# Performance work log

Measured on AMD Instinct MI355X. Metric: run time of the kernel, lower is better.

## Reference

```python
import jax, jax.numpy as jnp
import numpy as np

B, T, P, L, H = 65536, 256, 4, 14, 32
IN = P + L  # 18


def setup_inputs() -> dict:
    key = jax.random.key(0)
    ks = jax.random.split(key, 8)
    s1 = 1.0 / np.sqrt(IN)
    s2 = 1.0 / np.sqrt(H)
    return {
        "phys": jax.random.normal(ks[0], (B, T, P), dtype=jnp.float32),
        "latents": jax.random.normal(ks[1], (B, L), dtype=jnp.float32),
        "W1": jax.random.uniform(ks[2], (IN, H), jnp.float32, -s1, s1),
        "b1": jax.random.uniform(ks[3], (H,), jnp.float32, -s1, s1),
        "W2": jax.random.uniform(ks[4], (H, H), jnp.float32, -s2, s2),
        "b2": jax.random.uniform(ks[5], (H,), jnp.float32, -s2, s2),
        "W3": jax.random.uniform(ks[6], (H, L), jnp.float32, -s2, s2),
        "b3": jax.random.uniform(ks[7], (L,), jnp.float32, -s2, s2),
    }


def reference(phys, latents, W1, b1, W2, b2, W3, b3):
    # phys: [B, T, P]; latents: [B, L]. Dropout p=0.0 -> identity (eval-equivalent).
    phys_t = jnp.swapaxes(phys, 0, 1)  # [T, B, P] for scan over time

    def step(lat, ph):
        x = jnp.concatenate([ph, lat], axis=1)          # [B, P+L]
        h = jax.nn.relu(x @ W1 + b1)                    # [B, H]
        h = jax.nn.relu(h @ W2 + b2)                    # [B, H]
        lat = lat + (h @ W3 + b3)                       # residual update [B, L]
        return lat, lat

    _, outs = jax.lax.scan(step, latents, phys_t)       # outs: [T, B, L]
    return jnp.swapaxes(outs, 0, 1)                     # [B, T, L]
```

## Files before the change

### kernel.cpp

```cpp
#include <hip/hip_runtime.h>


#define BB 65536
#define TT 256
#define LL 14
#define HH 32

typedef float f32x16 __attribute__((ext_vector_type(16)));
typedef __bf16 bf16x8 __attribute__((ext_vector_type(8)));
typedef int i32x2 __attribute__((ext_vector_type(2)));

static __device__ __forceinline__ void split2(float v0, float v1,
                                              unsigned& hw, unsigned& lw) {
    unsigned u0 = __float_as_uint(v0), u1 = __float_as_uint(v1);
    unsigned h0 = (u0 + 0x8000u) & 0xFFFF0000u;
    unsigned h1 = (u1 + 0x8000u) & 0xFFFF0000u;
    float l0 = v0 - __uint_as_float(h0);
    float l1 = v1 - __uint_as_float(h1);
    unsigned s0 = __float_as_uint(l0), s1 = __float_as_uint(l1);
    hw = (h0 >> 16) | h1;
    lw = ((s0 + 0x8000u) >> 16) | ((s1 + 0x8000u) & 0xFFFF0000u);
}

static __device__ __forceinline__ bf16x8 mkfrag(unsigned w0, unsigned w1,
                                                unsigned w2, unsigned w3) {
    union { unsigned u[4]; bf16x8 v; } x;
    x.u[0] = w0; x.u[1] = w1; x.u[2] = w2; x.u[3] = w3;
    return x.v;
}

static __device__ __forceinline__ f32x16 mf(bf16x8 a, bf16x8 b, f32x16 c) {
    return __builtin_amdgcn_mfma_f32_32x32x16_bf16(a, b, c, 0, 0, 0);
}

#if __has_builtin(__builtin_amdgcn_permlane32_swap)
static __device__ __forceinline__ void xswap(unsigned a, unsigned b,
                                             unsigned& a_out, unsigned& b_out) {
    i32x2 r = __builtin_amdgcn_permlane32_swap((int)a, (int)b, false, false);
    a_out = (unsigned)r[0];
    b_out = (unsigned)r[1];
}
#else
static __device__ __forceinline__ void xswap(unsigned a, unsigned b,
                                             unsigned& a_out, unsigned& b_out) {
    const int lane = threadIdx.x & 63;
    const int idx = (lane ^ 32) << 2;
    unsigned sa = (unsigned)__builtin_amdgcn_ds_bpermute(idx, (int)a);
    unsigned sb = (unsigned)__builtin_amdgcn_ds_bpermute(idx, (int)b);
    const bool hi = lane >= 32;
    a_out = hi ? sb : a;
    b_out = hi ? b : sa;
}
#endif

static __device__ __forceinline__ void hfrag(const f32x16& h,
                                             bf16x8& B0h, bf16x8& B0l,
                                             bf16x8& B1h, bf16x8& B1l) {
    unsigned Wh[8], Wl[8];
#pragma unroll
    for (int p = 0; p < 8; ++p) split2(h[2 * p], h[2 * p + 1], Wh[p], Wl[p]);
    unsigned a02h, b02h, a02l, b02l, a13h, b13h, a13l, b13l;
    xswap(Wh[0], Wh[2], a02h, b02h); xswap(Wl[0], Wl[2], a02l, b02l);
    xswap(Wh[1], Wh[3], a13h, b13h); xswap(Wl[1], Wl[3], a13l, b13l);
    B0h = mkfrag(a02h, a13h, b02h, b13h);
    B0l = mkfrag(a02l, a13l, b02l, b13l);
    unsigned a46h, b46h, a46l, b46l, a57h, b57h, a57l, b57l;
    xswap(Wh[4], Wh[6], a46h, b46h); xswap(Wl[4], Wl[6], a46l, b46l);
    xswap(Wh[5], Wh[7], a57h, b57h); xswap(Wl[5], Wl[7], a57l, b57l);
    B1h = mkfrag(a46h, a57h, b46h, b57h);
    B1l = mkfrag(a46l, a57l, b46l, b57l);
}

__global__ __launch_bounds__(256, 2)
void emulator_kernel(const float* __restrict__ phys,
                     const float* __restrict__ latents,
                     const float* __restrict__ W1g,
                     const float* __restrict__ b1g,
                     const float* __restrict__ W2g,
                     const float* __restrict__ b2g,
                     const float* __restrict__ W3g,
                     const float* __restrict__ b3g,
                     float* __restrict__ out) {
    const int tid = threadIdx.x;
    const int lane = tid & 63;
    const int wv = tid >> 6;
    const int c = lane & 31;
    const bool hi = lane >= 32;
    const int kb = hi ? 8 : 0;
    const int r = blockIdx.x * 128 + wv * 32 + c;

    bf16x8 A1t0h, A1t0l, A1c;
    {
        unsigned hw[4], lw[4];
#pragma unroll
        for (int w = 0; w < 4; ++w) {
            const int k0 = kb + 2 * w;
            split2(W1g[k0 * HH + c], W1g[(k0 + 1) * HH + c], hw[w], lw[w]);
        }
        A1t0h = mkfrag(hw[0], hw[1], hw[2], hw[3]);
        A1t0l = mkfrag(lw[0], lw[1], lw[2], lw[3]);
        unsigned whp, wlp;
        split2(W1g[16 * HH + c], W1g[17 * HH + c], whp, wlp);
        A1c = hi ? mkfrag(0, 0, 0, 0) : mkfrag(whp, whp, wlp, 0);
    }
    bf16x8 A2h0, A2l0, A2h1, A2l1, A3h0, A3l0, A3h1, A3l1;
    {
        unsigned hw[4], lw[4];
#pragma unroll
        for (int w = 0; w < 4; ++w) {
            const int k0 = kb + 2 * w;
            split2(W2g[k0 * HH + c], W2g[(k0 + 1) * HH + c], hw[w], lw[w]);
        }
        A2h0 = mkfrag(hw[0], hw[1], hw[2], hw[3]);
        A2l0 = mkfrag(lw[0], lw[1], lw[2], lw[3]);
#pragma unroll
        for (int w = 0; w < 4; ++w) {
            const int k0 = 16 + kb + 2 * w;
            split2(W2g[k0 * HH + c], W2g[(k0 + 1) * HH + c], hw[w], lw[w]);
        }
        A2h1 = mkfrag(hw[0], hw[1], hw[2], hw[3]);
        A2l1 = mkfrag(lw[0], lw[1], lw[2], lw[3]);
#pragma unroll
        for (int w = 0; w < 4; ++w) {
            const int k0 = kb + 2 * w;
            const float e0 = (c < LL) ? W3g[k0 * LL + c] : 0.0f;
            const float e1 = (c < LL) ? W3g[(k0 + 1) * LL + c] : 0.0f;
            split2(e0, e1, hw[w], lw[w]);
        }
        A3h0 = mkfrag(hw[0], hw[1], hw[2], hw[3]);
        A3l0 = mkfrag(lw[0], lw[1], lw[2], lw[3]);
#pragma unroll
        for (int w = 0; w < 4; ++w) {
            const int k0 = 16 + kb + 2 * w;
            const float e0 = (c < LL) ? W3g[k0 * LL + c] : 0.0f;
            const float e1 = (c < LL) ? W3g[(k0 + 1) * LL + c] : 0.0f;
            split2(e0, e1, hw[w], lw[w]);
        }
        A3h1 = mkfrag(hw[0], hw[1], hw[2], hw[3]);
        A3l1 = mkfrag(lw[0], lw[1], lw[2], lw[3]);
    }

    f32x16 cb1, cb2, cb3;
#pragma unroll
    for (int rr = 0; rr < 16; ++rr) {
        const int row = (rr & 3) + 8 * (rr >> 2) + (hi ? 4 : 0);
        cb1[rr] = b1g[row];
        cb2[rr] = b2g[row];
        cb3[rr] = (row < LL) ? b3g[row] : 0.0f;
    }

    f32x16 lat;
#pragma unroll
    for (int i = 0; i < 16; ++i) lat[i] = 0.0f;
    {
        const float* lrow = latents + (size_t)r * LL;
        const float2* p01 = reinterpret_cast<const float2*>(lrow + (hi ? 4 : 0));
        const float2 v0 = p01[0], v1 = p01[1];
        lat[0] = v0.x; lat[1] = v0.y; lat[2] = v1.x; lat[3] = v1.y;
        const float2 v2 = reinterpret_cast<const float2*>(lrow + (hi ? 12 : 8))[0];
        lat[4] = v2.x; lat[5] = v2.y;
        if (!hi) {
            const float2 v3 = reinterpret_cast<const float2*>(lrow + 10)[0];
            lat[6] = v3.x; lat[7] = v3.y;
        }
    }

    const float4* pv = reinterpret_cast<const float4*>(phys) + (size_t)r * TT;
    float4 ph = pv[0];
    float* outr = out + (size_t)r * TT * LL;

#pragma unroll 1
    for (int t = 0; t < TT; ++t) {
        asm volatile("" : "+v"(A1t0h), "+v"(A1t0l), "+v"(A1c),
                          "+v"(A2h0), "+v"(A2l0), "+v"(A2h1), "+v"(A2l1),
                          "+v"(A3h0), "+v"(A3l0), "+v"(A3h1), "+v"(A3l1));
        asm volatile("" : "+v"(cb1), "+v"(cb2), "+v"(cb3));

        const float4 phn = pv[(t < TT - 1) ? (t + 1) : t];

        unsigned X0h, X0l, X1h, X1l, X2h, X2l, X3h, X3l, P0h, P0l, P1h, P1l;
        split2(lat[0], lat[1], X0h, X0l);
        split2(lat[2], lat[3], X1h, X1l);
        split2(lat[4], lat[5], X2h, X2l);
        split2(lat[6], lat[7], X3h, X3l);
        split2(ph.x, ph.y, P0h, P0l);
        split2(ph.z, ph.w, P1h, P1l);
        unsigned a2h, b2h, a2l, b2l, a3h, b3h, a3l, b3l;
        xswap(X2h, X2h, a2h, b2h); xswap(X2l, X2l, a2l, b2l);
        xswap(X3h, X3h, a3h, b3h); xswap(X3l, X3l, a3l, b3l);
        bf16x8 B0h = mkfrag(hi ? X0h : P0h, hi ? X1h : P1h,
                            hi ? a2h : X0h, hi ? a3h : X1h);
        bf16x8 B0l = mkfrag(hi ? X0l : P0l, hi ? X1l : P1l,
                            hi ? a2l : X0l, hi ? a3l : X1l);
        bf16x8 B1c = mkfrag(b2h, b2l, b2h, 0);

        f32x16 acc = mf(A1t0l, B0h, mf(A1t0h, B0l, mf(A1t0h, B0h, cb1)));
        acc = mf(A1c, B1c, acc);
        f32x16 h1v;
#pragma unroll
        for (int i = 0; i < 16; ++i) h1v[i] = fmaxf(acc[i], 0.0f);

        bf16x8 C0h, C0l, C1h, C1l;
        hfrag(h1v, C0h, C0l, C1h, C1l);
        f32x16 acc2 = mf(A2l0, C0h, mf(A2h0, C0l, mf(A2h0, C0h, cb2)));
        acc2 = mf(A2l1, C1h, mf(A2h1, C1l, mf(A2h1, C1h, acc2)));
        f32x16 h2v;
#pragma unroll
        for (int i = 0; i < 16; ++i) h2v[i] = fmaxf(acc2[i], 0.0f);

        bf16x8 D0h, D0l, D1h, D1l;
        hfrag(h2v, D0h, D0l, D1h, D1l);
        f32x16 c3;
#pragma unroll
        for (int i = 0; i < 16; ++i) c3[i] = lat[i] + cb3[i];
        f32x16 nl = mf(A3l0, D0h, mf(A3h0, D0l, mf(A3h0, D0h, c3)));
        nl = mf(A3l1, D1h, mf(A3h1, D1l, mf(A3h1, D1h, nl)));
        lat = nl;

        float* ob = outr + (size_t)t * LL;
        const int o0 = hi ? 4 : 0;
        *reinterpret_cast<float2*>(ob + o0)     = make_float2(lat[0], lat[1]);
        *reinterpret_cast<float2*>(ob + o0 + 2) = make_float2(lat[2], lat[3]);
        *reinterpret_cast<float2*>(ob + (hi ? 12 : 8)) = make_float2(lat[4], lat[5]);
        if (!hi)
            *reinterpret_cast<float2*>(ob + 10) = make_float2(lat[6], lat[7]);

        ph = phn;
    }
}

extern "C" void kernel_launch(void* const* d_in, const int* in_sizes, int n_in,
                              void* d_out, int out_size, void* d_ws, size_t ws_size,
                              hipStream_t stream) {
    const float* phys    = (const float*)d_in[0];
    const float* latents = (const float*)d_in[1];
    const float* W1      = (const float*)d_in[2];
    const float* b1      = (const float*)d_in[3];
    const float* W2      = (const float*)d_in[4];
    const float* b2      = (const float*)d_in[5];
    const float* W3      = (const float*)d_in[6];
    const float* b3      = (const float*)d_in[7];
    float* out = (float*)d_out;

    const int threads = 256;
    const int blocks = BB / 128;
    emulator_kernel<<<blocks, threads, 0, stream>>>(
        phys, latents, W1, b1, W2, b2, W3, b3, out);
}
```

Measured before the change: 629.2 us.

## Split MFMA accumulation chains into parallel halves, add setprio, use native bf16 converts

Each layer's serial chain of six dependent MFMAs becomes two independent three-MFMA chains, one starting from a zero accumulator, whose results are summed with VALU adds. Independent chains let the matrix pipe overlap instructions instead of waiting on each accumulator dependency. The MFMA groups are wrapped in s_setprio raises to favour this wave's issue. The hand-written bf16 hi/lo split is replaced with native bf16 conversions, which may lower to hardware convert instructions. This adds extra VALU adds, a zero register block, and slightly different rounding order.

After: 600.4 us. -4.6%, faster.

```diff
diff --git a/kernel.cpp b/kernel.cpp
--- a/kernel.cpp
+++ b/kernel.cpp
@@ -8,18 +8,23 @@
 
 typedef float f32x16 __attribute__((ext_vector_type(16)));
 typedef __bf16 bf16x8 __attribute__((ext_vector_type(8)));
+typedef __bf16 bf16x2 __attribute__((ext_vector_type(2)));
 typedef int i32x2 __attribute__((ext_vector_type(2)));
+
+static __device__ __forceinline__ unsigned packbf(float a, float b) {
+    bf16x2 p;
+    p[0] = (__bf16)a;
+    p[1] = (__bf16)b;
+    return __builtin_bit_cast(unsigned, p);
+}
 
 static __device__ __forceinline__ void split2(float v0, float v1,
                                               unsigned& hw, unsigned& lw) {
-    unsigned u0 = __float_as_uint(v0), u1 = __float_as_uint(v1);
-    unsigned h0 = (u0 + 0x8000u) & 0xFFFF0000u;
-    unsigned h1 = (u1 + 0x8000u) & 0xFFFF0000u;
-    float l0 = v0 - __uint_as_float(h0);
-    float l1 = v1 - __uint_as_float(h1);
-    unsigned s0 = __float_as_uint(l0), s1 = __float_as_uint(l1);
-    hw = (h0 >> 16) | h1;
-    lw = ((s0 + 0x8000u) >> 16) | ((s1 + 0x8000u) & 0xFFFF0000u);
+    const __bf16 h0 = (__bf16)v0, h1 = (__bf16)v1;
+    hw = packbf(v0, v1);
+    const float l0 = v0 - (float)h0;
+    const float l1 = v1 - (float)h1;
+    lw = packbf(l0, l1);
 }
 
 static __device__ __forceinline__ bf16x8 mkfrag(unsigned w0, unsigned w1,
@@ -140,13 +145,14 @@
         A3l1 = mkfrag(lw[0], lw[1], lw[2], lw[3]);
     }
 
-    f32x16 cb1, cb2, cb3;
+    f32x16 cb1, cb2, cb3, z;
 #pragma unroll
     for (int rr = 0; rr < 16; ++rr) {
         const int row = (rr & 3) + 8 * (rr >> 2) + (hi ? 4 : 0);
         cb1[rr] = b1g[row];
         cb2[rr] = b2g[row];
         cb3[rr] = (row < LL) ? b3g[row] : 0.0f;
+        z[rr] = 0.0f;
     }
 
     f32x16 lat;
@@ -173,8 +179,8 @@
     for (int t = 0; t < TT; ++t) {
         asm volatile("" : "+v"(A1t0h), "+v"(A1t0l), "+v"(A1c),
                           "+v"(A2h0), "+v"(A2l0), "+v"(A2h1), "+v"(A2l1),
-                          "+v"(A3h0), "+v"(A3l0), "+v"(A3h1), "+v"(A3l1));
-        asm volatile("" : "+v"(cb1), "+v"(cb2), "+v"(cb3));
+                          "+v"(A3h0), "+v"(A3l0), "+v"(A3h1), "+v"(A3l1),
+                          "+v"(cb1), "+v"(cb2), "+v"(cb3), "+v"(z));
 
         const float4 phn = pv[(t < TT - 1) ? (t + 1) : t];
 
@@ -194,28 +200,35 @@
                             hi ? a2l : X0l, hi ? a3l : X1l);
         bf16x8 B1c = mkfrag(b2h, b2l, b2h, 0);
 
-        f32x16 acc = mf(A1t0l, B0h, mf(A1t0h, B0l, mf(A1t0h, B0h, cb1)));
-        acc = mf(A1c, B1c, acc);
+        __builtin_amdgcn_s_setprio(1);
+        f32x16 accA = mf(A1t0l, B0h, mf(A1t0h, B0l, mf(A1t0h, B0h, cb1)));
+        f32x16 accB = mf(A1c, B1c, z);
+        __builtin_amdgcn_s_setprio(0);
         f32x16 h1v;
 #pragma unroll
-        for (int i = 0; i < 16; ++i) h1v[i] = fmaxf(acc[i], 0.0f);
+        for (int i = 0; i < 16; ++i) h1v[i] = fmaxf(accA[i] + accB[i], 0.0f);
 
         bf16x8 C0h, C0l, C1h, C1l;
         hfrag(h1v, C0h, C0l, C1h, C1l);
-        f32x16 acc2 = mf(A2l0, C0h, mf(A2h0, C0l, mf(A2h0, C0h, cb2)));
-        acc2 = mf(A2l1, C1h, mf(A2h1, C1l, mf(A2h1, C1h, acc2)));
+        __builtin_amdgcn_s_setprio(1);
+        f32x16 a2A = mf(A2l0, C0h, mf(A2h0, C0l, mf(A2h0, C0h, cb2)));
+        f32x16 a2B = mf(A2l1, C1h, mf(A2h1, C1l, mf(A2h1, C1h, z)));
+        __builtin_amdgcn_s_setprio(0);
         f32x16 h2v;
 #pragma unroll
-        for (int i = 0; i < 16; ++i) h2v[i] = fmaxf(acc2[i], 0.0f);
+        for (int i = 0; i < 16; ++i) h2v[i] = fmaxf(a2A[i] + a2B[i], 0.0f);
 
         bf16x8 D0h, D0l, D1h, D1l;
         hfrag(h2v, D0h, D0l, D1h, D1l);
         f32x16 c3;
 #pragma unroll
         for (int i = 0; i < 16; ++i) c3[i] = lat[i] + cb3[i];
-        f32x16 nl = mf(A3l0, D0h, mf(A3h0, D0l, mf(A3h0, D0h, c3)));
-        nl = mf(A3l1, D1h, mf(A3h1, D1l, mf(A3h1, D1h, nl)));
-        lat = nl;
+        __builtin_amdgcn_s_setprio(1);
+        f32x16 nlA = mf(A3l0, D0h, mf(A3h0, D0l, mf(A3h0, D0h, c3)));
+        f32x16 nlB = mf(A3l1, D1h, mf(A3h1, D1l, mf(A3h1, D1h, z)));
+        __builtin_amdgcn_s_setprio(0);
+#pragma unroll
+        for (int i = 0; i < 16; ++i) lat[i] = nlA[i] + nlB[i];
 
         float* ob = outr + (size_t)t * LL;
         const int o0 = hi ? 4 : 0;
```
